# Optimization experiments

Measured on AMD Instinct MI355X. Metric: run time of the kernel, lower is better.

The kernel has to match this reference:

```python
import jax, jax.numpy as jnp
import numpy as np

B, S, D, T = 32, 2048, 128, 8  # batch, seq, input_size, num_trans


def setup_inputs() -> dict:
    key = jax.random.key(0)
    k0, k1, k2, k3 = jax.random.split(key, 4)
    return {
        "input_data": jax.random.normal(k0, (B, S, D), dtype=jnp.float32),
        # nn.Linear(D, D) weights per transform, stacked: [T, D, D]
        "Wx": jax.random.normal(k1, (T, D, D), dtype=jnp.float32) / np.sqrt(D).astype(np.float32),
        "bx": jax.random.normal(k2, (T, D), dtype=jnp.float32) * 0.01,
        # torch.rand init in original
        "p_vectors": jax.random.uniform(k3, (T, 1, D), dtype=jnp.float32),
    }


def reference(input_data, Wx, bx, p_vectors):
    # Batched version of the Python loop of per-transform Linears.
    # torch Linear computes x @ W.T + b -> contract last dim of x with last dim of W.
    transformed = jnp.einsum('bsd,ted->tbse', input_data, Wx) + bx[:, None, None, :]  # [T,B,S,D]

    # Cosine-similarity gating against prototype vectors p_vectors [T,1,D].
    x_norm = jnp.linalg.norm(input_data, axis=2, keepdims=True)[None]        # [1,B,S,1]
    p_norm = jnp.linalg.norm(p_vectors, axis=2, keepdims=True)[:, None]      # [T,1,1,1]
    dot = jnp.sum(input_data[None] * p_vectors[:, None], axis=3, keepdims=True)  # [T,B,S,1]
    cos = dot / (x_norm * p_norm)
    sim = jax.nn.softmax(cos, axis=0)  # softmax over the T transforms

    # Weighted combine + residual (is_y=False path).
    return jnp.sum(sim * transformed, axis=0) + input_data  # [B,S,D]
```

## Files before the change

kernel.cpp:

```cpp
#include <hip/hip_runtime.h>

#define Bq 32
#define Sq 2048
#define Dq 128
#define Tq 8
#define Mq (Bq * Sq)

typedef __attribute__((ext_vector_type(8))) short bf16x8;
typedef __attribute__((ext_vector_type(4))) float f32x4;

static __device__ __forceinline__ unsigned short f2bf(float f) {
    unsigned int u = __float_as_uint(f);
    unsigned int r = (u + 0x7FFFu + ((u >> 16) & 1u)) >> 16;
    return (unsigned short)r;
}

__global__ void prep_kernel(const float* __restrict__ W, unsigned short* __restrict__ wsw) {
    int i = blockIdx.x * 256 + threadIdx.x;
    int j    = i & 7;
    int lane = (i >> 3) & 63;
    int k    = (i >> 9) & 3;
    int n    = (i >> 11) & 7;
    int t    = i >> 14;
    int e = n * 16 + (lane & 15);
    int d = k * 32 + (lane >> 4) * 8 + j;
    float w = W[(t * 128 + e) * 128 + d];
    if (e == d) w += 1.0f;
    wsw[i] = f2bf(w);
}

__global__ __launch_bounds__(256, 2) void main_kernel(const float* __restrict__ x,
                                                      const unsigned short* __restrict__ wsw,
                                                      const float* __restrict__ bx,
                                                      const float* __restrict__ p,
                                                      float* __restrict__ out) {
    __shared__ unsigned short xs[128][136];
    __shared__ float simT[Tq][128];
    __shared__ float bxl[Tq][128];
    __shared__ f32x4 p4[Tq][32];
    __shared__ float pinv[Tq];

    int tid = threadIdx.x;
    size_t m0 = (size_t)blockIdx.x * 128;

    int r = tid >> 1;
    int h = tid & 1;

    const f32x4* xg = reinterpret_cast<const f32x4*>(x + (m0 + r) * 128) + h * 16;
    f32x4 xv[16];
    #pragma unroll
    for (int j = 0; j < 16; j++) xv[j] = __builtin_nontemporal_load(xg + j);

    reinterpret_cast<f32x4*>(&p4[0][0])[tid] = reinterpret_cast<const f32x4*>(p)[tid];
    reinterpret_cast<f32x4*>(&bxl[0][0])[tid] = reinterpret_cast<const f32x4*>(bx)[tid];
    if (tid < Tq) {
        const f32x4* pg = reinterpret_cast<const f32x4*>(p) + tid * 32;
        float s = 0.f;
        #pragma unroll
        for (int i = 0; i < 32; i++) {
            f32x4 v = pg[i];
            s += v.x * v.x + v.y * v.y + v.z * v.z + v.w * v.w;
        }
        pinv[tid] = rsqrtf(s);
    }
    __syncthreads();

    float dot[Tq];
    #pragma unroll
    for (int t = 0; t < Tq; t++) dot[t] = 0.f;
    float ssq = 0.f;
    #pragma unroll
    for (int j = 0; j < 16; j++) {
        f32x4 v = xv[j];
        ssq += v.x * v.x + v.y * v.y + v.z * v.z + v.w * v.w;
        #pragma unroll
        for (int t = 0; t < Tq; t++) {
            f32x4 pv = p4[t][h * 16 + j];
            dot[t] += v.x * pv.x + v.y * pv.y + v.z * pv.z + v.w * pv.w;
        }
    }
    #pragma unroll
    for (int jj = 0; jj < 8; jj++) {
        f32x4 v0 = xv[2 * jj], v1 = xv[2 * jj + 1];
        bf16x8 b;
        b[0] = (short)f2bf(v0.x); b[1] = (short)f2bf(v0.y);
        b[2] = (short)f2bf(v0.z); b[3] = (short)f2bf(v0.w);
        b[4] = (short)f2bf(v1.x); b[5] = (short)f2bf(v1.y);
        b[6] = (short)f2bf(v1.z); b[7] = (short)f2bf(v1.w);
        *reinterpret_cast<bf16x8*>(&xs[r][h * 64 + jj * 8]) = b;
    }
    ssq += __shfl_xor(ssq, 1);
    #pragma unroll
    for (int t = 0; t < Tq; t++) dot[t] += __shfl_xor(dot[t], 1);
    float xinv = rsqrtf(ssq);
    float c[Tq], mx = -1e30f;
    #pragma unroll
    for (int t = 0; t < Tq; t++) {
        c[t] = dot[t] * xinv * pinv[t];
        mx = fmaxf(mx, c[t]);
    }
    float sum = 0.f;
    #pragma unroll
    for (int t = 0; t < Tq; t++) { c[t] = __expf(c[t] - mx); sum += c[t]; }
    float inv = 1.f / sum;
    #pragma unroll
    for (int i = 0; i < 4; i++) simT[h * 4 + i][r] = c[h * 4 + i] * inv;
    __syncthreads();

    int wid  = tid >> 6;
    int lane = tid & 63;
    int l16  = lane & 15;
    int quad = lane >> 4;
    int mrow = (wid >> 1) * 64;
    int ncol = (wid & 1) * 64;
    int nt0  = ncol >> 4;

    bf16x8 a[4][4];
    #pragma unroll
    for (int mt = 0; mt < 4; mt++)
        #pragma unroll
        for (int k = 0; k < 4; k++)
            a[mt][k] = *reinterpret_cast<const bf16x8*>(&xs[mrow + mt * 16 + l16][k * 32 + quad * 8]);

    f32x4 o[4][4] = {};

    const bf16x8* wbase = reinterpret_cast<const bf16x8*>(wsw);
    bf16x8 bf[2][4];
    #pragma unroll
    for (int k = 0; k < 4; k++)
        bf[0][k] = wbase[((size_t)(0 * 8 + nt0) * 4 + k) * 64 + lane];

    #pragma unroll 1
    for (int t = 0; t < Tq; t++) {
        f32x4 s[4];
        #pragma unroll
        for (int mt = 0; mt < 4; mt++)
            s[mt] = *reinterpret_cast<const f32x4*>(&simT[t][mrow + mt * 16 + quad * 4]);

        #pragma unroll
        for (int n = 0; n < 4; n++) {
            const int cur = n & 1;
            {
                const int n2 = (n + 1) & 3;
                int t2 = (n == 3) ? ((t + 1) & 7) : t;
                #pragma unroll
                for (int k = 0; k < 4; k++)
                    bf[cur ^ 1][k] = wbase[((size_t)(t2 * 8 + nt0 + n2) * 4 + k) * 64 + lane];
            }
            f32x4 y[4] = {};
            #pragma unroll
            for (int k = 0; k < 4; k++)
                #pragma unroll
                for (int mt = 0; mt < 4; mt++)
                    y[mt] = __builtin_amdgcn_mfma_f32_16x16x32_bf16(a[mt][k], bf[cur][k], y[mt], 0, 0, 0);
            float bias = bxl[t][ncol + n * 16 + l16];
            #pragma unroll
            for (int mt = 0; mt < 4; mt++)
                #pragma unroll
                for (int rr = 0; rr < 4; rr++)
                    o[mt][n][rr] += s[mt][rr] * (y[mt][rr] + bias);
        }
    }

    #pragma unroll
    for (int mt = 0; mt < 4; mt++)
        #pragma unroll
        for (int rr = 0; rr < 4; rr++) {
            size_t row = m0 + mrow + mt * 16 + quad * 4 + rr;
            #pragma unroll
            for (int n = 0; n < 4; n++) {
                size_t idx = row * 128 + ncol + n * 16 + l16;
                __builtin_nontemporal_store(o[mt][n][rr], out + idx);
            }
        }
}

extern "C" void kernel_launch(void* const* d_in, const int* in_sizes, int n_in,
                              void* d_out, int out_size, void* d_ws, size_t ws_size,
                              hipStream_t stream) {
    const float* x   = (const float*)d_in[0];
    const float* Wx  = (const float*)d_in[1];
    const float* bx  = (const float*)d_in[2];
    const float* p   = (const float*)d_in[3];
    float* out = (float*)d_out;

    unsigned short* wsw = (unsigned short*)d_ws;

    prep_kernel<<<dim3(512), dim3(256), 0, stream>>>(Wx, wsw);
    main_kernel<<<dim3(Mq / 128), dim3(256), 0, stream>>>(x, wsw, bx, p, out);
}
```

Before: 119.6 us.

## Halve row tile to 64 and restructure MFMA loop k-outer with bias-initialized accumulators

Each block now handles 64 rows instead of 128, with four threads per row for the norm and dot prologue. Each wave computes a 32x64 tile with its transform output held in registers for all four column tiles at once. The k loop now sits outermost and prefetches weight fragments per k step. Accumulators start from the bias, and launch bounds rise to 3 blocks per CU to raise occupancy and latency hiding. In exchange, every 64 rows reload the full weight set, which doubles weight traffic from L2, and each wave gets less reuse per weight fragment.

```diff
diff --git a/kernel.cpp b/kernel.cpp
--- a/kernel.cpp
+++ b/kernel.cpp
@@ -29,27 +29,27 @@
     wsw[i] = f2bf(w);
 }
 
-__global__ __launch_bounds__(256, 2) void main_kernel(const float* __restrict__ x,
+__global__ __launch_bounds__(256, 3) void main_kernel(const float* __restrict__ x,
                                                       const unsigned short* __restrict__ wsw,
                                                       const float* __restrict__ bx,
                                                       const float* __restrict__ p,
                                                       float* __restrict__ out) {
-    __shared__ unsigned short xs[128][136];
-    __shared__ float simT[Tq][128];
+    __shared__ unsigned short xs[64][136];
+    __shared__ float simT[Tq][64];
     __shared__ float bxl[Tq][128];
     __shared__ f32x4 p4[Tq][32];
     __shared__ float pinv[Tq];
 
     int tid = threadIdx.x;
-    size_t m0 = (size_t)blockIdx.x * 128;
-
-    int r = tid >> 1;
-    int h = tid & 1;
-
-    const f32x4* xg = reinterpret_cast<const f32x4*>(x + (m0 + r) * 128) + h * 16;
-    f32x4 xv[16];
-    #pragma unroll
-    for (int j = 0; j < 16; j++) xv[j] = __builtin_nontemporal_load(xg + j);
+    size_t m0 = (size_t)blockIdx.x * 64;
+
+    int r = tid >> 2;
+    int h = tid & 3;
+
+    const f32x4* xg = reinterpret_cast<const f32x4*>(x + (m0 + r) * 128) + h * 8;
+    f32x4 xv[8];
+    #pragma unroll
+    for (int j = 0; j < 8; j++) xv[j] = __builtin_nontemporal_load(xg + j);
 
     reinterpret_cast<f32x4*>(&p4[0][0])[tid] = reinterpret_cast<const f32x4*>(p)[tid];
     reinterpret_cast<f32x4*>(&bxl[0][0])[tid] = reinterpret_cast<const f32x4*>(bx)[tid];
@@ -70,28 +70,31 @@
     for (int t = 0; t < Tq; t++) dot[t] = 0.f;
     float ssq = 0.f;
     #pragma unroll
-    for (int j = 0; j < 16; j++) {
+    for (int j = 0; j < 8; j++) {
         f32x4 v = xv[j];
         ssq += v.x * v.x + v.y * v.y + v.z * v.z + v.w * v.w;
         #pragma unroll
         for (int t = 0; t < Tq; t++) {
-            f32x4 pv = p4[t][h * 16 + j];
+            f32x4 pv = p4[t][h * 8 + j];
             dot[t] += v.x * pv.x + v.y * pv.y + v.z * pv.z + v.w * pv.w;
         }
     }
     #pragma unroll
-    for (int jj = 0; jj < 8; jj++) {
+    for (int jj = 0; jj < 4; jj++) {
         f32x4 v0 = xv[2 * jj], v1 = xv[2 * jj + 1];
         bf16x8 b;
         b[0] = (short)f2bf(v0.x); b[1] = (short)f2bf(v0.y);
         b[2] = (short)f2bf(v0.z); b[3] = (short)f2bf(v0.w);
         b[4] = (short)f2bf(v1.x); b[5] = (short)f2bf(v1.y);
         b[6] = (short)f2bf(v1.z); b[7] = (short)f2bf(v1.w);
-        *reinterpret_cast<bf16x8*>(&xs[r][h * 64 + jj * 8]) = b;
-    }
-    ssq += __shfl_xor(ssq, 1);
-    #pragma unroll
-    for (int t = 0; t < Tq; t++) dot[t] += __shfl_xor(dot[t], 1);
+        *reinterpret_cast<bf16x8*>(&xs[r][h * 32 + jj * 8]) = b;
+    }
+    ssq += __shfl_xor(ssq, 1); ssq += __shfl_xor(ssq, 2);
+    #pragma unroll
+    for (int t = 0; t < Tq; t++) {
+        dot[t] += __shfl_xor(dot[t], 1);
+        dot[t] += __shfl_xor(dot[t], 2);
+    }
     float xinv = rsqrtf(ssq);
     float c[Tq], mx = -1e30f;
     #pragma unroll
@@ -103,67 +106,74 @@
     #pragma unroll
     for (int t = 0; t < Tq; t++) { c[t] = __expf(c[t] - mx); sum += c[t]; }
     float inv = 1.f / sum;
-    #pragma unroll
-    for (int i = 0; i < 4; i++) simT[h * 4 + i][r] = c[h * 4 + i] * inv;
+    simT[2 * h][r]     = c[2 * h] * inv;
+    simT[2 * h + 1][r] = c[2 * h + 1] * inv;
     __syncthreads();
 
     int wid  = tid >> 6;
     int lane = tid & 63;
     int l16  = lane & 15;
     int quad = lane >> 4;
-    int mrow = (wid >> 1) * 64;
+    int mrow = (wid >> 1) * 32;
     int ncol = (wid & 1) * 64;
-    int nt0  = ncol >> 4;
-
-    bf16x8 a[4][4];
-    #pragma unroll
-    for (int mt = 0; mt < 4; mt++)
+    int nt0  = (wid & 1) * 4;
+
+    bf16x8 a[2][4];
+    #pragma unroll
+    for (int mt = 0; mt < 2; mt++)
         #pragma unroll
         for (int k = 0; k < 4; k++)
             a[mt][k] = *reinterpret_cast<const bf16x8*>(&xs[mrow + mt * 16 + l16][k * 32 + quad * 8]);
 
-    f32x4 o[4][4] = {};
+    f32x4 o[2][4] = {};
 
     const bf16x8* wbase = reinterpret_cast<const bf16x8*>(wsw);
     bf16x8 bf[2][4];
     #pragma unroll
-    for (int k = 0; k < 4; k++)
-        bf[0][k] = wbase[((size_t)(0 * 8 + nt0) * 4 + k) * 64 + lane];
+    for (int n = 0; n < 4; n++)
+        bf[0][n] = wbase[((size_t)(0 * 8 + nt0 + n) * 4 + 0) * 64 + lane];
 
     #pragma unroll 1
     for (int t = 0; t < Tq; t++) {
-        f32x4 s[4];
-        #pragma unroll
-        for (int mt = 0; mt < 4; mt++)
+        f32x4 s[2];
+        #pragma unroll
+        for (int mt = 0; mt < 2; mt++)
             s[mt] = *reinterpret_cast<const f32x4*>(&simT[t][mrow + mt * 16 + quad * 4]);
 
+        f32x4 y[2][4];
         #pragma unroll
         for (int n = 0; n < 4; n++) {
-            const int cur = n & 1;
+            float bias = bxl[t][ncol + n * 16 + l16];
+            y[0][n] = (f32x4){bias, bias, bias, bias};
+            y[1][n] = (f32x4){bias, bias, bias, bias};
+        }
+
+        #pragma unroll
+        for (int k = 0; k < 4; k++) {
             {
-                const int n2 = (n + 1) & 3;
-                int t2 = (n == 3) ? ((t + 1) & 7) : t;
+                int kn = (k + 1) & 3;
+                int tn = (k == 3) ? ((t + 1) & 7) : t;
                 #pragma unroll
-                for (int k = 0; k < 4; k++)
-                    bf[cur ^ 1][k] = wbase[((size_t)(t2 * 8 + nt0 + n2) * 4 + k) * 64 + lane];
+                for (int n = 0; n < 4; n++)
+                    bf[(k + 1) & 1][n] = wbase[((size_t)(tn * 8 + nt0 + n) * 4 + kn) * 64 + lane];
             }
-            f32x4 y[4] = {};
             #pragma unroll
-            for (int k = 0; k < 4; k++)
+            for (int n = 0; n < 4; n++)
                 #pragma unroll
-                for (int mt = 0; mt < 4; mt++)
-                    y[mt] = __builtin_amdgcn_mfma_f32_16x16x32_bf16(a[mt][k], bf[cur][k], y[mt], 0, 0, 0);
-            float bias = bxl[t][ncol + n * 16 + l16];
+                for (int mt = 0; mt < 2; mt++)
+                    y[mt][n] = __builtin_amdgcn_mfma_f32_16x16x32_bf16(a[mt][k], bf[k & 1][n], y[mt][n], 0, 0, 0);
+        }
+        #pragma unroll
+        for (int mt = 0; mt < 2; mt++)
             #pragma unroll
-            for (int mt = 0; mt < 4; mt++)
+            for (int n = 0; n < 4; n++)
                 #pragma unroll
                 for (int rr = 0; rr < 4; rr++)
-                    o[mt][n][rr] += s[mt][rr] * (y[mt][rr] + bias);
-        }
-    }
-
-    #pragma unroll
-    for (int mt = 0; mt < 4; mt++)
+                    o[mt][n][rr] += s[mt][rr] * y[mt][n][rr];
+    }
+
+    #pragma unroll
+    for (int mt = 0; mt < 2; mt++)
         #pragma unroll
         for (int rr = 0; rr < 4; rr++) {
             size_t row = m0 + mrow + mt * 16 + quad * 4 + rr;
@@ -187,5 +197,5 @@
     unsigned short* wsw = (unsigned short*)d_ws;
 
     prep_kernel<<<dim3(512), dim3(256), 0, stream>>>(Wx, wsw);
-    main_kernel<<<dim3(Mq / 128), dim3(256), 0, stream>>>(x, wsw, bx, p, out);
-}
+    main_kernel<<<dim3(Mq / 64), dim3(256), 0, stream>>>(x, wsw, bx, p, out);
+}
```

Measured after the change: 139.8 us. 1.17x slower.
